# Kernel optimization log

Measured on AMD Instinct MI355X. Metric: run time of the kernel, lower is better.

Reference implementation:

```python
import jax, jax.numpy as jnp
import numpy as np
from jax import lax

INPUT, HIDDEN, LAYERS, ACTIONS = 512, 128, 2, 10
B, T = 512, 256


def _lstm_layer(x_seq, Wih, Whh, bih, bhh):
    """x_seq: [B,T,D] -> (outputs [B,T,H], h_T [B,H], c_T [B,H]). PyTorch gate order i,f,g,o."""
    Bsz = x_seq.shape[0]
    H = Whh.shape[1]
    # Precompute input projection for all timesteps (one big GEMM).
    x_proj = jnp.einsum('btd,gd->btg', x_seq, Wih) + bih + bhh  # [B,T,4H]

    def step(carry, xt):
        h, c = carry
        gates = xt + h @ Whh.T  # [B,4H]
        i, f, g, o = jnp.split(gates, 4, axis=-1)
        c = jax.nn.sigmoid(f) * c + jax.nn.sigmoid(i) * jnp.tanh(g)
        h = jax.nn.sigmoid(o) * jnp.tanh(c)
        return (h, c), h

    init = (jnp.zeros((Bsz, H), x_seq.dtype), jnp.zeros((Bsz, H), x_seq.dtype))
    (hT, cT), hs = lax.scan(step, init, jnp.swapaxes(x_proj, 0, 1))  # hs: [T,B,H]
    return jnp.swapaxes(hs, 0, 1), hT, cT


def setup_inputs() -> dict:
    key = jax.random.key(0)
    ks = jax.random.split(key, 16)
    s_in = 1.0 / np.sqrt(HIDDEN)

    def u(k, shape):
        return jax.random.uniform(k, shape, jnp.float32, -s_in, s_in)

    return {
        'x': jax.random.normal(ks[0], (B, T, INPUT), jnp.float32),
        'Wih0': u(ks[1], (4 * HIDDEN, INPUT)),
        'Whh0': u(ks[2], (4 * HIDDEN, HIDDEN)),
        'bih0': u(ks[3], (4 * HIDDEN,)),
        'bhh0': u(ks[4], (4 * HIDDEN,)),
        'Wih1': u(ks[5], (4 * HIDDEN, HIDDEN)),
        'Whh1': u(ks[6], (4 * HIDDEN, HIDDEN)),
        'bih1': u(ks[7], (4 * HIDDEN,)),
        'bhh1': u(ks[8], (4 * HIDDEN,)),
        'fc1_w': u(ks[9], (HIDDEN // 2, HIDDEN)),
        'fc1_b': u(ks[10], (HIDDEN // 2,)),
        'fc2_w': u(ks[11], (ACTIONS, HIDDEN // 2)),
        'fc2_b': u(ks[12], (ACTIONS,)),
    }


def reference(x, Wih0, Whh0, bih0, bhh0, Wih1, Whh1, bih1, bhh1, fc1_w, fc1_b, fc2_w, fc2_b):
    # Layer 0 (input 512 -> hidden 128); dropout is inference-off (identity).
    h0_seq, h0, c0 = _lstm_layer(x, Wih0, Whh0, bih0, bhh0)
    # Layer 1 (hidden 128 -> hidden 128)
    h1_seq, h1, c1 = _lstm_layer(h0_seq, Wih1, Whh1, bih1, bhh1)
    last = h1_seq[:, -1, :]  # [B,H]
    hid = jax.nn.relu(last @ fc1_w.T + fc1_b)
    logits = hid @ fc2_w.T + fc2_b
    probs = jax.nn.softmax(logits, axis=-1)
    h_n = jnp.stack([h0, h1], axis=0)  # [num_layers,B,H]
    c_n = jnp.stack([c0, c1], axis=0)
    return probs, h_n, c_n
```

## Files before the change

kernel.cpp:

```cpp
#include <hip/hip_runtime.h>
#include <hip/hip_bf16.h>


#define BATCH 512
#define SEQT  256
#define INPUTD 512
#define HID   128
#define GATES 512
#define RB    4
#define SUBS  16
#define NCH   (SEQT / SUBS)

typedef __bf16 bf16_t;
typedef bf16_t bf16x4 __attribute__((ext_vector_type(4)));
typedef bf16_t bf16x8 __attribute__((ext_vector_type(8)));
typedef float  f32x4  __attribute__((ext_vector_type(4)));

__device__ __forceinline__ float sigm(float x) {
    return __builtin_amdgcn_rcpf(1.f + __expf(-x));
}
__device__ __forceinline__ float tanhfast(float x) {
    float xc = fminf(fmaxf(x, -15.f), 15.f);
    float e = __expf(2.f * xc);
    return (e - 1.f) * __builtin_amdgcn_rcpf(e + 1.f);
}

__global__ __launch_bounds__(256) void cvt_weights(
    const float* __restrict__ w0, const float* __restrict__ w1,
    const float* __restrict__ w2, const float* __restrict__ w3,
    bf16_t* __restrict__ o0, bf16_t* __restrict__ o1,
    bf16_t* __restrict__ o2, bf16_t* __restrict__ o3,
    unsigned* __restrict__ flags)
{
    int b = blockIdx.x;
    if (b == 448) {
        uint4 z = make_uint4(0u, 0u, 0u, 0u);
        #pragma unroll
        for (int i = 0; i < 4; ++i)
            ((uint4*)flags)[i * 256 + threadIdx.x] = z;
        return;
    }
    const float* src; bf16_t* dst; long base;
    if (b < 256)      { src = w0; dst = o0; base = (long)b * 256; }
    else if (b < 320) { src = w1; dst = o1; base = (long)(b - 256) * 256; }
    else if (b < 384) { src = w2; dst = o2; base = (long)(b - 320) * 256; }
    else              { src = w3; dst = o3; base = (long)(b - 384) * 256; }
    long i = base + threadIdx.x;
    float4 v = ((const float4*)src)[i];
    bf16x4 r;
    r[0] = (bf16_t)v.x; r[1] = (bf16_t)v.y;
    r[2] = (bf16_t)v.z; r[3] = (bf16_t)v.w;
    ((bf16x4*)dst)[i] = r;
}

__global__ __launch_bounds__(256) void gemm_mfma(
    const float* __restrict__ A, const bf16_t* __restrict__ W,
    const float* __restrict__ b1, const float* __restrict__ b2,
    float* __restrict__ out,
    int K, int tcs, int tcmask, int srcT, int t0)
{
    __shared__ bf16_t As[128 * 32];
    __shared__ bf16_t Bs[128 * 32];
    int tid = threadIdx.x;
    int l = tid & 63;
    int w = tid >> 6;
    int wm = w >> 1, wn = w & 1;
    int bn = blockIdx.x;
    int bm = blockIdx.y;
    int Tc = tcmask + 1;

    long aoff[2], boff[2];
    #pragma unroll
    for (int c = 0; c < 2; ++c) {
        int m = bm * 128 + (tid >> 2) + 64 * c;
        int xr = ((m >> tcs) * srcT) + t0 + (m & tcmask);
        aoff[c] = (long)xr * K + (tid & 3) * 8;
        int n = bn * 128 + (tid >> 2) + 64 * c;
        boff[c] = (long)n * K + (tid & 3) * 8;
    }

    f32x4 acc[4][4];
    #pragma unroll
    for (int i = 0; i < 4; ++i)
        #pragma unroll
        for (int j = 0; j < 4; ++j)
            acc[i][j] = (f32x4){0.f, 0.f, 0.f, 0.f};

    const int rbase = wm * 64 + (l & 15);
    const int cbase = wn * 64 + (l & 15);
    const int kfrag = (l >> 4) * 8;

    for (int kt = 0; kt < K; kt += 32) {
        float4 av[2][2];
        #pragma unroll
        for (int c = 0; c < 2; ++c) {
            av[c][0] = *(const float4*)(A + aoff[c] + kt);
            av[c][1] = *(const float4*)(A + aoff[c] + kt + 4);
        }
        __builtin_amdgcn_global_load_lds(
            (const __attribute__((address_space(1))) void*)(W + boff[0] + kt),
            (__attribute__((address_space(3))) void*)(Bs + tid * 8), 16, 0, 0);
        __builtin_amdgcn_global_load_lds(
            (const __attribute__((address_space(1))) void*)(W + boff[1] + kt),
            (__attribute__((address_space(3))) void*)(Bs + 2048 + tid * 8), 16, 0, 0);
        #pragma unroll
        for (int c = 0; c < 2; ++c) {
            bf16x8 ab;
            ab[0] = (bf16_t)av[c][0].x; ab[1] = (bf16_t)av[c][0].y;
            ab[2] = (bf16_t)av[c][0].z; ab[3] = (bf16_t)av[c][0].w;
            ab[4] = (bf16_t)av[c][1].x; ab[5] = (bf16_t)av[c][1].y;
            ab[6] = (bf16_t)av[c][1].z; ab[7] = (bf16_t)av[c][1].w;
            *(bf16x8*)(As + c * 2048 + tid * 8) = ab;
        }
        __syncthreads();

        bf16x8 af[4], bfr[4];
        #pragma unroll
        for (int i = 0; i < 4; ++i)
            af[i] = *(const bf16x8*)(As + (rbase + i * 16) * 32 + kfrag);
        #pragma unroll
        for (int j = 0; j < 4; ++j)
            bfr[j] = *(const bf16x8*)(Bs + (cbase + j * 16) * 32 + kfrag);

        #pragma unroll
        for (int i = 0; i < 4; ++i)
            #pragma unroll
            for (int j = 0; j < 4; ++j)
                acc[i][j] = __builtin_amdgcn_mfma_f32_16x16x32_bf16(
                    af[i], bfr[j], acc[i][j], 0, 0, 0);
        __syncthreads();
    }

    #pragma unroll
    for (int i = 0; i < 4; ++i) {
        int m0 = bm * 128 + wm * 64 + i * 16 + (l >> 4) * 4;
        #pragma unroll
        for (int j = 0; j < 4; ++j) {
            int n = bn * 128 + wn * 64 + j * 16 + (l & 15);
            float bb = b1[n] + b2[n];
            int hid = n & 127;
            #pragma unroll
            for (int r = 0; r < 4; ++r) {
                int m = m0 + r;
                int b = m >> tcs;
                int t = m & tcmask;
                int br = b >> 2, brow = b & 3;
                out[(((long)br * Tc + t) * 4 + bn) * 512 + brow * 128 + hid] =
                    acc[i][j][r] + bb;
            }
        }
    }
}

#define BARRIER_()                                                             \
    do {                                                                       \
        asm volatile("s_waitcnt lgkmcnt(0)" ::: "memory");                     \
        __builtin_amdgcn_s_barrier();                                          \
        __builtin_amdgcn_sched_barrier(0);                                     \
    } while (0)

#define REC0_STEP(X, t)                                                        \
    {                                                                          \
        bf16x8 a[4];                                                           \
        _Pragma("unroll")                                                      \
        for (int ks = 0; ks < 4; ++ks) {                                       \
            int ba = (col * 256 + ks * 64 + lgroup * 16) ^ ((col & 7) << 4);   \
            a[ks] = *(const bf16x8*)((const char*)h_lds + ba);                 \
        }                                                                      \
        f32x4 acc[4];                                                          \
        _Pragma("unroll")                                                      \
        for (int g = 0; g < 4; ++g) acc[g] = (f32x4){0.f, 0.f, 0.f, 0.f};      \
        _Pragma("unroll")                                                      \
        for (int ks = 0; ks < 4; ++ks)                                         \
            _Pragma("unroll")                                                  \
            for (int g = 0; g < 4; ++g)                                        \
                acc[g] = __builtin_amdgcn_mfma_f32_16x16x32_bf16(              \
                    a[ks], __builtin_bit_cast(bf16x8, wreg[g][ks]), acc[g],    \
                    0, 0, 0);                                                  \
        if (lgroup == 0) {                                                     \
            _Pragma("unroll")                                                  \
            for (int r = 0; r < 4; ++r) {                                      \
                f32x4 v;                                                       \
                v[0] = acc[0][r]; v[1] = acc[1][r];                            \
                v[2] = acc[2][r]; v[3] = acc[3][r];                            \
                *(f32x4*)((char*)g_lds + r * 2048 + coff * 16) = v;            \
            }                                                                  \
        }                                                                      \
        BARRIER_();                                                            \
        {                                                                      \
            f32x4 gv = *(const f32x4*)((const char*)g_lds + tid * 16);         \
            float zi = gv[0] + X.x, zf = gv[1] + X.y;                          \
            float zg = gv[2] + X.z, zo = gv[3] + X.w;                          \
            c = sigm(zf) * c + sigm(zi) * tanhfast(zg);                        \
            h = sigm(zo) * tanhfast(c);                                        \
            *(bf16_t*)((char*)h_lds + hba) = (bf16_t)h;                        \
            h0qp[(long)(t) * 512] = (bf16_t)h;                                 \
        }                                                                      \
        if ((t) + 2 < Tc) {                                                    \
            long o = (long)((t) + 2) * 2048;                                   \
            X.x = xpt[o];        X.y = xpt[o + 512];                           \
            X.z = xpt[o + 1024]; X.w = xpt[o + 1536];                          \
        }                                                                      \
        if (((t) & (SUBS - 1)) == SUBS - 1)                                    \
            asm volatile("s_waitcnt vmcnt(0)" ::: "memory");                   \
        BARRIER_();                                                            \
        if ((((t) & (SUBS - 1)) == SUBS - 1) && tid == 0) {                    \
            __threadfence();                                                   \
            __hip_atomic_store(flagp + ((t) >> 4), 1u, __ATOMIC_RELEASE,       \
                               __HIP_MEMORY_SCOPE_AGENT);                      \
        }                                                                      \
    }

__global__ __launch_bounds__(512, 2) void lstm_dual(
    const float* __restrict__ xp4,
    const bf16_t* __restrict__ Wh0,
    const bf16_t* __restrict__ Wi1,
    const bf16_t* __restrict__ Wh1,
    const float* __restrict__ bih1, const float* __restrict__ bhh1,
    bf16_t* __restrict__ h0q,
    unsigned* __restrict__ flags,
    float* __restrict__ h0st, float* __restrict__ c0st,
    float* __restrict__ h1st, float* __restrict__ c1st,
    int Tc, int first, int subbase)
{
    __shared__ __align__(16) char pool[28 * 1024];
    int tid = threadIdx.x;
    int l = tid & 63;
    int wv = tid >> 6;
    int pair = blockIdx.x & 127;
    int r0 = pair * RB;
    int col = l & 15;
    int lgroup = l >> 4;
    int kreg = lgroup * 8;
    int coff = wv * 16 + col;
    int erow = tid >> 7, ehid = tid & 127;
    const int hba = (erow * 256 + ehid * 2) ^ ((erow & 7) << 4);
    unsigned* flagp = flags + pair * NCH + subbase;

    if (blockIdx.x < 128) {
        bf16_t* h_lds = (bf16_t*)pool;
        float*  g_lds = (float*)(pool + 4096);

        f32x4 wreg[4][4];
        #pragma unroll
        for (int g = 0; g < 4; ++g)
            #pragma unroll
            for (int ks = 0; ks < 4; ++ks)
                wreg[g][ks] = *(const f32x4*)(Wh0 + (long)(g * 128 + coff) * HID
                                              + ks * 32 + kreg);
        #pragma unroll
        for (int g = 0; g < 4; ++g)
            #pragma unroll
            for (int ks = 0; ks < 4; ++ks)
                asm volatile("" : "+a"(wreg[g][ks]));

        float c = first ? 0.f : c0st[(r0 + erow) * HID + ehid];
        float h = first ? 0.f : h0st[(r0 + erow) * HID + ehid];

        ((float2*)h_lds)[tid & 255] = make_float2(0.f, 0.f);
        __syncthreads();
        *(bf16_t*)((char*)h_lds + hba) = (bf16_t)h;
        __syncthreads();

        const float* xpt = xp4 + (long)pair * Tc * 2048 + tid;
        bf16_t* h0qp = h0q + (long)pair * Tc * 512 + (hba >> 1);
        float4 xA, xB;
        xA.x = xpt[0];    xA.y = xpt[512];
        xA.z = xpt[1024]; xA.w = xpt[1536];
        if (Tc > 1) {
            xB.x = xpt[2048];        xB.y = xpt[2048 + 512];
            xB.z = xpt[2048 + 1024]; xB.w = xpt[2048 + 1536];
        } else {
            xB = make_float4(0.f, 0.f, 0.f, 0.f);
        }

        for (int tt = 0; tt < Tc; tt += 2) {
            REC0_STEP(xA, tt)
            REC0_STEP(xB, tt + 1)
        }

        h0st[(r0 + erow) * HID + ehid] = h;
        c0st[(r0 + erow) * HID + ehid] = c;
    } else {
        bf16_t* h0stg = (bf16_t*)pool;
        bf16_t* h1_lds = (bf16_t*)(pool + 16384);
        float*  g_lds = (float*)(pool + 20480);

        f32x4 wI[4][4], wH[4][4];
        #pragma unroll
        for (int g = 0; g < 4; ++g)
            #pragma unroll
            for (int ks = 0; ks < 4; ++ks) {
                long o = (long)(g * 128 + coff) * HID + ks * 32 + kreg;
                wI[g][ks] = *(const f32x4*)(Wi1 + o);
                wH[g][ks] = *(const f32x4*)(Wh1 + o);
            }
        #pragma unroll
        for (int g = 0; g < 4; ++g)
            #pragma unroll
            for (int ks = 0; ks < 4; ++ks) {
                asm volatile("" : "+a"(wI[g][ks]));
                asm volatile("" : "+a"(wH[g][ks]));
            }

        float4 bias1;
        bias1.x = bih1[ehid]       + bhh1[ehid];
        bias1.y = bih1[128 + ehid] + bhh1[128 + ehid];
        bias1.z = bih1[256 + ehid] + bhh1[256 + ehid];
        bias1.w = bih1[384 + ehid] + bhh1[384 + ehid];

        float c1 = first ? 0.f : c1st[(r0 + erow) * HID + ehid];
        float h1 = first ? 0.f : h1st[(r0 + erow) * HID + ehid];

        #pragma unroll
        for (int i = 0; i < 5; ++i)
            ((float2*)pool)[i * 512 + tid] = make_float2(0.f, 0.f);
        __syncthreads();
        *(bf16_t*)((char*)h1_lds + hba) = (bf16_t)h1;
        __syncthreads();

        if (wv == 0) {
            while (__hip_atomic_load(flagp, __ATOMIC_ACQUIRE,
                                     __HIP_MEMORY_SCOPE_AGENT) == 0u)
                __builtin_amdgcn_s_sleep(2);
            __builtin_amdgcn_global_load_lds(
                (const __attribute__((address_space(1))) void*)(
                    h0q + (long)pair * Tc * 512 + l * 8),
                (__attribute__((address_space(3))) void*)h0stg, 16, 0, 0);
            if (Tc > 1)
                __builtin_amdgcn_global_load_lds(
                    (const __attribute__((address_space(1))) void*)(
                        h0q + ((long)pair * Tc + 1) * 512 + l * 8),
                    (__attribute__((address_space(3))) void*)(h0stg + 2048),
                    16, 0, 0);
            asm volatile("s_waitcnt vmcnt(0)" ::: "memory");
        }
        __syncthreads();

        for (int t = 0; t < Tc; ++t) {
            if (t + 2 < Tc && wv == (t & 3)) {
                if (((t + 2) & (SUBS - 1)) == 0) {
                    unsigned* fp = flagp + ((t + 2) >> 4);
                    while (__hip_atomic_load(fp, __ATOMIC_ACQUIRE,
                                             __HIP_MEMORY_SCOPE_AGENT) == 0u)
                        __builtin_amdgcn_s_sleep(2);
                }
                __builtin_amdgcn_global_load_lds(
                    (const __attribute__((address_space(1))) void*)(
                        h0q + ((long)pair * Tc + t + 2) * 512 + l * 8),
                    (__attribute__((address_space(3))) void*)(
                        h0stg + ((t + 2) & 3) * 2048), 16, 0, 0);
            }

            const char* sb = (const char*)h0stg + (t & 3) * 4096;
            bf16x8 a0[4], a1[4];
            #pragma unroll
            for (int ks = 0; ks < 4; ++ks) {
                int ba = (col * 256 + ks * 64 + lgroup * 16) ^ ((col & 7) << 4);
                a0[ks] = *(const bf16x8*)(sb + ba);
                a1[ks] = *(const bf16x8*)((const char*)h1_lds + ba);
            }
            f32x4 acc[4];
            #pragma unroll
            for (int g = 0; g < 4; ++g) acc[g] = (f32x4){0.f, 0.f, 0.f, 0.f};
            #pragma unroll
            for (int ks = 0; ks < 4; ++ks)
                #pragma unroll
                for (int g = 0; g < 4; ++g)
                    acc[g] = __builtin_amdgcn_mfma_f32_16x16x32_bf16(
                        a0[ks], __builtin_bit_cast(bf16x8, wI[g][ks]), acc[g],
                        0, 0, 0);
            #pragma unroll
            for (int ks = 0; ks < 4; ++ks)
                #pragma unroll
                for (int g = 0; g < 4; ++g)
                    acc[g] = __builtin_amdgcn_mfma_f32_16x16x32_bf16(
                        a1[ks], __builtin_bit_cast(bf16x8, wH[g][ks]), acc[g],
                        0, 0, 0);
            if (lgroup == 0) {
                #pragma unroll
                for (int r = 0; r < 4; ++r) {
                    f32x4 v;
                    v[0] = acc[0][r]; v[1] = acc[1][r];
                    v[2] = acc[2][r]; v[3] = acc[3][r];
                    *(f32x4*)((char*)g_lds + r * 2048 + coff * 16) = v;
                }
            }
            BARRIER_();

            {
                f32x4 gv = *(const f32x4*)((const char*)g_lds + tid * 16);
                float zi = gv[0] + bias1.x;
                float zf = gv[1] + bias1.y;
                float zg = gv[2] + bias1.z;
                float zo = gv[3] + bias1.w;
                c1 = sigm(zf) * c1 + sigm(zi) * tanhfast(zg);
                h1 = sigm(zo) * tanhfast(c1);
                *(bf16_t*)((char*)h1_lds + hba) = (bf16_t)h1;
            }
            if (t + 1 < Tc && wv == ((t + 3) & 3))
                asm volatile("s_waitcnt vmcnt(0)" ::: "memory");
            BARRIER_();
        }

        h1st[(r0 + erow) * HID + ehid] = h1;
        c1st[(r0 + erow) * HID + ehid] = c1;
    }
}

__global__ __launch_bounds__(128) void fc_head(
    const float* __restrict__ h0st, const float* __restrict__ c0st,
    const float* __restrict__ h1st, const float* __restrict__ c1st,
    const float* __restrict__ fc1w, const float* __restrict__ fc1b,
    const float* __restrict__ fc2w, const float* __restrict__ fc2b,
    float* __restrict__ out)
{
    __shared__ float h1_s[HID];
    __shared__ float hid_s[64];
    __shared__ float log_s[10];
    int t = threadIdx.x;
    int b = blockIdx.x;

    h1_s[t] = h1st[b * HID + t];
    __syncthreads();

    if (t < 64) {
        float a = fc1b[t];
        const float* wrow = fc1w + t * HID;
        #pragma unroll 4
        for (int k = 0; k < HID; ++k) a = fmaf(wrow[k], h1_s[k], a);
        hid_s[t] = fmaxf(a, 0.f);
    }
    __syncthreads();

    if (t < 10) {
        float a = fc2b[t];
        const float* wrow = fc2w + t * 64;
        #pragma unroll 4
        for (int k = 0; k < 64; ++k) a = fmaf(wrow[k], hid_s[k], a);
        log_s[t] = a;
    }
    __syncthreads();

    if (t == 0) {
        float m = log_s[0];
        #pragma unroll
        for (int j = 1; j < 10; ++j) m = fmaxf(m, log_s[j]);
        float e[10];
        float s = 0.f;
        #pragma unroll
        for (int j = 0; j < 10; ++j) { e[j] = __expf(log_s[j] - m); s += e[j]; }
        float inv = __builtin_amdgcn_rcpf(s);
        #pragma unroll
        for (int j = 0; j < 10; ++j) out[b * 10 + j] = e[j] * inv;
    }

    float* hn = out + BATCH * 10;
    float* cn = hn + 2 * BATCH * HID;
    hn[b * HID + t] = h0st[b * HID + t];
    hn[BATCH * HID + b * HID + t] = h1_s[t];
    cn[b * HID + t] = c0st[b * HID + t];
    cn[BATCH * HID + b * HID + t] = c1st[b * HID + t];
}

extern "C" void kernel_launch(void* const* d_in, const int* in_sizes, int n_in,
                              void* d_out, int out_size, void* d_ws, size_t ws_size,
                              hipStream_t stream) {
    const float* x    = (const float*)d_in[0];
    const float* Wih0 = (const float*)d_in[1];
    const float* Whh0 = (const float*)d_in[2];
    const float* bih0 = (const float*)d_in[3];
    const float* bhh0 = (const float*)d_in[4];
    const float* Wih1 = (const float*)d_in[5];
    const float* Whh1 = (const float*)d_in[6];
    const float* bih1 = (const float*)d_in[7];
    const float* bhh1 = (const float*)d_in[8];
    const float* fc1w = (const float*)d_in[9];
    const float* fc1b = (const float*)d_in[10];
    const float* fc2w = (const float*)d_in[11];
    const float* fc2b = (const float*)d_in[12];
    float* out = (float*)d_out;

    int Tc = SEQT;
    while (Tc > SUBS) {
        size_t need = (size_t)BATCH * Tc * GATES * 4
                    + ((size_t)GATES * INPUTD + 3 * (size_t)GATES * HID) * 2
                    + (size_t)128 * Tc * 512 * 2
                    + 4 * (size_t)BATCH * HID * 4
                    + 128 * NCH * 4 + 512;
        if (need <= ws_size) break;
        Tc >>= 1;
    }
    int tcs = __builtin_ctz((unsigned)Tc);

    float*    xp   = (float*)d_ws;
    bf16_t*   wb0  = (bf16_t*)(xp + (size_t)BATCH * Tc * GATES);
    bf16_t*   wb1  = wb0 + (size_t)GATES * INPUTD;
    bf16_t*   wh0b = wb1 + (size_t)GATES * HID;
    bf16_t*   wh1b = wh0b + (size_t)GATES * HID;
    bf16_t*   h0q  = wh1b + (size_t)GATES * HID;
    float*    h0st = (float*)(h0q + (size_t)128 * Tc * 512);
    float*    c0st = h0st + (size_t)BATCH * HID;
    float*    h1st = c0st + (size_t)BATCH * HID;
    float*    c1st = h1st + (size_t)BATCH * HID;
    unsigned* flags = (unsigned*)(c1st + (size_t)BATCH * HID);

    cvt_weights<<<449, 256, 0, stream>>>(Wih0, Wih1, Whh0, Whh1,
                                         wb0, wb1, wh0b, wh1b, flags);

    int nchunk = SEQT / Tc;
    dim3 gemm_grid(GATES / 128, (BATCH * Tc) / 128);

    for (int ci = 0; ci < nchunk; ++ci) {
        gemm_mfma<<<gemm_grid, 256, 0, stream>>>(
            x, wb0, bih0, bhh0, xp, INPUTD, tcs, Tc - 1, SEQT, ci * Tc);
        lstm_dual<<<256, 512, 0, stream>>>(
            xp, wh0b, wb1, wh1b, bih1, bhh1, h0q, flags,
            h0st, c0st, h1st, c1st, Tc, ci == 0, ci * (Tc / SUBS));
    }

    fc_head<<<BATCH, 128, 0, stream>>>(
        h0st, c0st, h1st, c1st, fc1w, fc1b, fc2w, fc2b, out);
}
```

Before: 568.7 us.

## Store layer-0 input projection in bf16 and split layer-1 MFMA accumulators

The precomputed input-projection buffer (B*T*4H) is now written by the GEMM as bf16 instead of fp32 and converted back to float when the recurrent kernel loads it, halving its footprint and traffic. Halving the size can also let a larger time chunk fit in the workspace, which means fewer chunk launches. Separately, the layer-1 recurrent step keeps two independent accumulator sets for the input and hidden MFMAs and interleaves them, which shortens the dependent MFMA chain. The cost is reduced precision in the pre-activations and more accumulator registers.

Measured after the change: 662.8 us. 1.17x slower.

```diff
diff --git a/kernel.cpp b/kernel.cpp
--- a/kernel.cpp
+++ b/kernel.cpp
@@ -56,7 +56,7 @@
 __global__ __launch_bounds__(256) void gemm_mfma(
     const float* __restrict__ A, const bf16_t* __restrict__ W,
     const float* __restrict__ b1, const float* __restrict__ b2,
-    float* __restrict__ out,
+    bf16_t* __restrict__ out,
     int K, int tcs, int tcmask, int srcT, int t0)
 {
     __shared__ bf16_t As[128 * 32];
@@ -146,7 +146,7 @@
                 int t = m & tcmask;
                 int br = b >> 2, brow = b & 3;
                 out[(((long)br * Tc + t) * 4 + bn) * 512 + brow * 128 + hid] =
-                    acc[i][j][r] + bb;
+                    (bf16_t)(acc[i][j][r] + bb);
             }
         }
     }
@@ -198,8 +198,8 @@
         }                                                                      \
         if ((t) + 2 < Tc) {                                                    \
             long o = (long)((t) + 2) * 2048;                                   \
-            X.x = xpt[o];        X.y = xpt[o + 512];                           \
-            X.z = xpt[o + 1024]; X.w = xpt[o + 1536];                          \
+            X.x = (float)xpt[o];        X.y = (float)xpt[o + 512];             \
+            X.z = (float)xpt[o + 1024]; X.w = (float)xpt[o + 1536];            \
         }                                                                      \
         if (((t) & (SUBS - 1)) == SUBS - 1)                                    \
             asm volatile("s_waitcnt vmcnt(0)" ::: "memory");                   \
@@ -212,7 +212,7 @@
     }
 
 __global__ __launch_bounds__(512, 2) void lstm_dual(
-    const float* __restrict__ xp4,
+    const bf16_t* __restrict__ xp4,
     const bf16_t* __restrict__ Wh0,
     const bf16_t* __restrict__ Wi1,
     const bf16_t* __restrict__ Wh1,
@@ -262,14 +262,14 @@
         *(bf16_t*)((char*)h_lds + hba) = (bf16_t)h;
         __syncthreads();
 
-        const float* xpt = xp4 + (long)pair * Tc * 2048 + tid;
+        const bf16_t* xpt = xp4 + (long)pair * Tc * 2048 + tid;
         bf16_t* h0qp = h0q + (long)pair * Tc * 512 + (hba >> 1);
         float4 xA, xB;
-        xA.x = xpt[0];    xA.y = xpt[512];
-        xA.z = xpt[1024]; xA.w = xpt[1536];
+        xA.x = (float)xpt[0];    xA.y = (float)xpt[512];
+        xA.z = (float)xpt[1024]; xA.w = (float)xpt[1536];
         if (Tc > 1) {
-            xB.x = xpt[2048];        xB.y = xpt[2048 + 512];
-            xB.z = xpt[2048 + 1024]; xB.w = xpt[2048 + 1536];
+            xB.x = (float)xpt[2048];        xB.y = (float)xpt[2048 + 512];
+            xB.z = (float)xpt[2048 + 1024]; xB.w = (float)xpt[2048 + 1536];
         } else {
             xB = make_float4(0.f, 0.f, 0.f, 0.f);
         }
@@ -360,29 +360,31 @@
                 a0[ks] = *(const bf16x8*)(sb + ba);
                 a1[ks] = *(const bf16x8*)((const char*)h1_lds + ba);
             }
-            f32x4 acc[4];
-            #pragma unroll
-            for (int g = 0; g < 4; ++g) acc[g] = (f32x4){0.f, 0.f, 0.f, 0.f};
+            f32x4 accI[4], accH[4];
+            #pragma unroll
+            for (int g = 0; g < 4; ++g) {
+                accI[g] = (f32x4){0.f, 0.f, 0.f, 0.f};
+                accH[g] = (f32x4){0.f, 0.f, 0.f, 0.f};
+            }
             #pragma unroll
             for (int ks = 0; ks < 4; ++ks)
                 #pragma unroll
-                for (int g = 0; g < 4; ++g)
-                    acc[g] = __builtin_amdgcn_mfma_f32_16x16x32_bf16(
-                        a0[ks], __builtin_bit_cast(bf16x8, wI[g][ks]), acc[g],
+                for (int g = 0; g < 4; ++g) {
+                    accI[g] = __builtin_amdgcn_mfma_f32_16x16x32_bf16(
+                        a0[ks], __builtin_bit_cast(bf16x8, wI[g][ks]), accI[g],
                         0, 0, 0);
-            #pragma unroll
-            for (int ks = 0; ks < 4; ++ks)
-                #pragma unroll
-                for (int g = 0; g < 4; ++g)
-                    acc[g] = __builtin_amdgcn_mfma_f32_16x16x32_bf16(
-                        a1[ks], __builtin_bit_cast(bf16x8, wH[g][ks]), acc[g],
+                    accH[g] = __builtin_amdgcn_mfma_f32_16x16x32_bf16(
+                        a1[ks], __builtin_bit_cast(bf16x8, wH[g][ks]), accH[g],
                         0, 0, 0);
+                }
             if (lgroup == 0) {
                 #pragma unroll
                 for (int r = 0; r < 4; ++r) {
                     f32x4 v;
-                    v[0] = acc[0][r]; v[1] = acc[1][r];
-                    v[2] = acc[2][r]; v[3] = acc[3][r];
+                    v[0] = accI[0][r] + accH[0][r];
+                    v[1] = accI[1][r] + accH[1][r];
+                    v[2] = accI[2][r] + accH[2][r];
+                    v[3] = accI[3][r] + accH[3][r];
                     *(f32x4*)((char*)g_lds + r * 2048 + coff * 16) = v;
                 }
             }
@@ -483,7 +485,7 @@
 
     int Tc = SEQT;
     while (Tc > SUBS) {
-        size_t need = (size_t)BATCH * Tc * GATES * 4
+        size_t need = (size_t)BATCH * Tc * GATES * 2
                     + ((size_t)GATES * INPUTD + 3 * (size_t)GATES * HID) * 2
                     + (size_t)128 * Tc * 512 * 2
                     + 4 * (size_t)BATCH * HID * 4
@@ -493,8 +495,8 @@
     }
     int tcs = __builtin_ctz((unsigned)Tc);
 
-    float*    xp   = (float*)d_ws;
-    bf16_t*   wb0  = (bf16_t*)(xp + (size_t)BATCH * Tc * GATES);
+    bf16_t*   xp   = (bf16_t*)d_ws;
+    bf16_t*   wb0  = xp + (size_t)BATCH * Tc * GATES;
     bf16_t*   wb1  = wb0 + (size_t)GATES * INPUTD;
     bf16_t*   wh0b = wb1 + (size_t)GATES * HID;
     bf16_t*   wh1b = wh0b + (size_t)GATES * HID;
```
